# Optimization experiments

Hardware: AMD Instinct MI355X
Metric: run time of the kernel (lower is better)

The kernel has to match this reference:

```python
import jax, jax.numpy as jnp
import numpy as np

N_NODES = 100000
N_EDGES = 3200000
FEAT = 16


def gcn_conv(x, src, dst, W, b):
    # PyG GCNConv: add self-loops, symmetric normalization deg^{-1/2}(A+I)deg^{-1/2},
    # then linear transform and scatter-add aggregation.
    n = x.shape[0]
    loop = jnp.arange(n, dtype=src.dtype)
    s = jnp.concatenate([src, loop])
    d = jnp.concatenate([dst, loop])
    deg = jax.ops.segment_sum(jnp.ones_like(d, dtype=x.dtype), d, num_segments=n)
    dinv = jnp.where(deg > 0, jax.lax.rsqrt(deg), 0.0)
    norm = dinv[s] * dinv[d]  # [E+N]
    h = x @ W  # [N, out]
    msg = h[s] * norm[:, None]  # gather + weight
    out = jax.ops.segment_sum(msg, d, num_segments=n)  # scatter-add
    return out + b


def setup_inputs() -> dict:
    key = jax.random.key(0)
    k1, k2, k3, k4 = jax.random.split(key, 4)
    scale = 1.0 / np.sqrt(FEAT)
    return {
        "x": jax.random.normal(k1, (N_NODES, FEAT), dtype=jnp.float32),
        "edge_index": jax.random.randint(k2, (2, N_EDGES), 0, N_NODES, dtype=jnp.int64) if jax.config.jax_enable_x64 else jax.random.randint(k2, (2, N_EDGES), 0, N_NODES, dtype=jnp.int32),
        "W1": jax.random.normal(k3, (FEAT, 16), dtype=jnp.float32) * scale,
        "b1": jnp.zeros((16,), dtype=jnp.float32),
        "W2": jax.random.normal(k4, (16, FEAT), dtype=jnp.float32) * scale,
        "b2": jnp.zeros((FEAT,), dtype=jnp.float32),
    }


def reference(x, edge_index, W1, b1, W2, b2):
    src, dst = edge_index[0], edge_index[1]
    h = gcn_conv(x, src, dst, W1, b1)
    h = jax.nn.relu(h)
    out = gcn_conv(h, src, dst, W2, b2)
    return out
```

## Files before the change

### kernel.cpp

```cpp
#include <hip/hip_runtime.h>

#define F 16
#define BSHIFT 8
#define NPB 256
#define NB 391
#define CH 4096
#define BCAP 9216


__global__ void init_cursor_kernel(unsigned* __restrict__ cursor) {
    int i = threadIdx.x;
    if (i < NB) cursor[i * 16] = (unsigned)(i * BCAP);
}

__global__ __launch_bounds__(512) void
reorder_kernel(const int* __restrict__ src, const int* __restrict__ dst,
               unsigned* __restrict__ cursor, unsigned* __restrict__ recs, int E) {
    __shared__ unsigned lsorted[CH];
    __shared__ unsigned short lbkt[CH];
    __shared__ unsigned cnt[NB];
    __shared__ unsigned lstart[NB + 1];
    int t = threadIdx.x, b = blockIdx.x;
    int e0 = b * CH;
    int cnt_e = E - e0; if (cnt_e > CH) cnt_e = CH;

    for (int i = t; i < NB; i += 512) cnt[i] = 0;
    __syncthreads();
    unsigned pk[8], rs[8];
#pragma unroll
    for (int j = 0; j < 8; ++j) {
        int i = t + j * 512;
        pk[j] = 0xFFFFFFFFu;
        if (i < cnt_e) {
            unsigned d = (unsigned)dst[e0 + i];
            rs[j] = (unsigned)src[e0 + i];
            unsigned bk = d >> BSHIFT;
            unsigned r = atomicAdd(&cnt[bk], 1u);
            pk[j] = bk | ((d & 255u) << 9) | (r << 17);
        }
    }
    __syncthreads();
    if (t < 64) {
        unsigned run = 0;
        for (int c = 0; c < NB; c += 64) {
            int idx = c + t;
            unsigned v = (idx < NB) ? cnt[idx] : 0u;
            unsigned inc = v;
#pragma unroll
            for (int d = 1; d < 64; d <<= 1) {
                unsigned o = __shfl_up(inc, d, 64);
                if (t >= d) inc += o;
            }
            if (idx < NB) lstart[idx] = run + inc - v;
            run += __shfl(inc, 63, 64);
        }
        if (t == 0) lstart[NB] = (unsigned)cnt_e;
    }
    __syncthreads();
    for (int i = t; i < NB; i += 512) {
        unsigned c = cnt[i];
        if (c) cnt[i] = atomicAdd(&cursor[i * 16], c);
    }
    __syncthreads();
#pragma unroll
    for (int j = 0; j < 8; ++j) {
        int i = t + j * 512;
        if (i < cnt_e) {
            unsigned p = pk[j];
            unsigned bk = p & 0x1FFu;
            unsigned pos = lstart[bk] + (p >> 17);
            lsorted[pos] = rs[j] | (((p >> 9) & 255u) << 17);
            lbkt[pos] = (unsigned short)bk;
        }
    }
    __syncthreads();
    for (int i = t; i < cnt_e; i += 512) {
        unsigned bk = lbkt[i];
        recs[cnt[bk] + ((unsigned)i - lstart[bk])] = lsorted[i];
    }
}

__global__ __launch_bounds__(1024) void
sort2_kernel(const unsigned* __restrict__ recs, const unsigned* __restrict__ cursor,
             unsigned* __restrict__ srcs, int* __restrict__ noff, int* __restrict__ nend,
             float* __restrict__ dinv, const float* __restrict__ x,
             float* __restrict__ z, int n) {
    __shared__ unsigned lsort[BCAP];
    __shared__ unsigned cnt[NPB];
    __shared__ unsigned ex[NPB];
    __shared__ float ldv[NPB];
    __shared__ unsigned wtot[4];
    int t = threadIdx.x, b = blockIdx.x;
    int e0 = b * BCAP;
    int used = (int)(cursor[b * 16] - (unsigned)e0);
    if (t < NPB) cnt[t] = 0;
    __syncthreads();
    unsigned pk[9], rsr[9];
#pragma unroll
    for (int j = 0; j < 9; ++j) {
        int i = t + j * 1024;
        pk[j] = 0xFFFFFFFFu;
        if (i < used) {
            unsigned rec = recs[e0 + i];
            unsigned node = rec >> 17;
            rsr[j] = rec & 0x1FFFFu;
            unsigned r = atomicAdd(&cnt[node], 1u);
            pk[j] = node | (r << 8);
        }
    }
    __syncthreads();
    if (t < NPB) {
        unsigned c = cnt[t];
        unsigned inc = c;
        int lane = t & 63, w = t >> 6;
#pragma unroll
        for (int d = 1; d < 64; d <<= 1) {
            unsigned o = __shfl_up(inc, d, 64);
            if (lane >= d) inc += o;
        }
        if (lane == 63) wtot[w] = inc;
        __syncthreads();
        unsigned wbase = 0;
        for (int i = 0; i < w; ++i) wbase += wtot[i];
        unsigned e = wbase + inc - c;
        ex[t] = e;
        float dv = rsqrtf((float)c + 1.0f);
        ldv[t] = dv;
        int node = b * NPB + t;
        if (node < n) {
            noff[node] = e0 + (int)e;
            nend[node] = e0 + (int)(e + c);
            dinv[node] = dv;
        }
    } else {
        __syncthreads();
    }
    __syncthreads();
#pragma unroll
    for (int j = 0; j < 9; ++j) {
        int i = t + j * 1024;
        if (i < used) {
            unsigned p = pk[j];
            lsort[ex[p & 255u] + (p >> 8)] = rsr[j];
        }
    }
    __syncthreads();
    for (int i = t; i < used; i += 1024) srcs[e0 + i] = lsort[i];
    {
        int node = b * NPB + (t >> 2);
        if (node < n) {
            float4 v = ((const float4*)x)[(size_t)b * 1024 + t];
            float dv = ldv[t >> 2];
            v.x *= dv; v.y *= dv; v.z *= dv; v.w *= dv;
            ((float4*)z)[(size_t)b * 1024 + t] = v;
        }
    }
}

__global__ void agg_csr_kernel(const float* __restrict__ hin, const unsigned* __restrict__ srcs,
                               const int* __restrict__ noff, const int* __restrict__ nend,
                               const float* __restrict__ dinv,
                               const float* __restrict__ W, const float* __restrict__ bias,
                               float* __restrict__ outp, int n, int mode) {
    __shared__ float a1[64][F + 1];
    __shared__ float Ws[F * F];
    int t = threadIdx.x;
    int g = t >> 2, c = t & 3;
    Ws[t] = W[t];
    int node = blockIdx.x * 64 + g;
    const float4* h4 = (const float4*)hin;
    float di = 0.f;
    if (node < n) {
        di = dinv[node];
        int e0 = noff[node], e1 = nend[node];
        float4 s0 = {0,0,0,0}, s1 = {0,0,0,0}, s2 = {0,0,0,0}, s3 = {0,0,0,0};
        int e = e0;
        for (; e + 4 <= e1; e += 4) {
            int ia = srcs[e], ib = srcs[e + 1], ic = srcs[e + 2], id = srcs[e + 3];
            float4 va = h4[(size_t)ia * 4 + c];
            float4 vb = h4[(size_t)ib * 4 + c];
            float4 vc = h4[(size_t)ic * 4 + c];
            float4 vd = h4[(size_t)id * 4 + c];
            s0.x += va.x; s0.y += va.y; s0.z += va.z; s0.w += va.w;
            s1.x += vb.x; s1.y += vb.y; s1.z += vb.z; s1.w += vb.w;
            s2.x += vc.x; s2.y += vc.y; s2.z += vc.z; s2.w += vc.w;
            s3.x += vd.x; s3.y += vd.y; s3.z += vd.z; s3.w += vd.w;
        }
        for (; e < e1; ++e) {
            float4 va = h4[(size_t)srcs[e] * 4 + c];
            s0.x += va.x; s0.y += va.y; s0.z += va.z; s0.w += va.w;
        }
        float4 self = h4[(size_t)node * 4 + c];
        a1[g][c * 4 + 0] = (s0.x + s1.x) + (s2.x + s3.x) + self.x;
        a1[g][c * 4 + 1] = (s0.y + s1.y) + (s2.y + s3.y) + self.y;
        a1[g][c * 4 + 2] = (s0.z + s1.z) + (s2.z + s3.z) + self.z;
        a1[g][c * 4 + 3] = (s0.w + s1.w) + (s2.w + s3.w) + self.w;
    }
    __syncthreads();
    if (node < n) {
        float4 o = {0.f, 0.f, 0.f, 0.f};
        int j = c * 4;
#pragma unroll
        for (int k = 0; k < F; ++k) {
            float ak = a1[g][k];
            o.x += ak * Ws[k * F + j + 0];
            o.y += ak * Ws[k * F + j + 1];
            o.z += ak * Ws[k * F + j + 2];
            o.w += ak * Ws[k * F + j + 3];
        }
        float4 bi = ((const float4*)bias)[c];
        o.x = di * o.x + bi.x; o.y = di * o.y + bi.y;
        o.z = di * o.z + bi.z; o.w = di * o.w + bi.w;
        if (mode == 1) {
            o.x = fmaxf(o.x, 0.f) * di; o.y = fmaxf(o.y, 0.f) * di;
            o.z = fmaxf(o.z, 0.f) * di; o.w = fmaxf(o.w, 0.f) * di;
        }
        ((float4*)outp)[(size_t)node * 4 + c] = o;
    }
}


__global__ void deg_kernel(const int* __restrict__ dst, float* __restrict__ deg, int E) {
    int e = blockIdx.x * blockDim.x + threadIdx.x;
    if (e < E) atomicAdd(&deg[dst[e]], 1.0f);
}
__global__ void dinv_kernel(float* __restrict__ deg, int n) {
    int i = blockIdx.x * blockDim.x + threadIdx.x;
    if (i < n) deg[i] = rsqrtf(deg[i] + 1.0f);
}
__global__ void linear2_kernel(const float* __restrict__ in, const float* __restrict__ acc,
                               const float* __restrict__ dinv, const float* __restrict__ W,
                               const float* __restrict__ bias, float* __restrict__ out,
                               int n, int mode) {
    __shared__ float Ws[F * F];
    __shared__ float As[16][F + 1];
    int t = threadIdx.x;
    Ws[t] = W[t];
    int nb = t >> 4, j = t & 15;
    int i = blockIdx.x * 16 + nb;
    float di = 0.f, v = 0.f;
    if (i < n) {
        di = dinv[i]; v = in[i * F + j];
        if (mode) { v = di * (acc[i * F + j] + v) + bias[j]; v = fmaxf(v, 0.f); }
    }
    As[nb][j] = v;
    __syncthreads();
    if (i < n) {
        float s = 0.f;
#pragma unroll
        for (int k = 0; k < F; ++k) s += As[nb][k] * Ws[k * F + j];
        out[i * F + j] = s * di;
    }
}
__global__ void scatter_kernel(const int* __restrict__ src, const int* __restrict__ dst,
                               const float* __restrict__ h, float* __restrict__ acc, int E) {
    int t = blockIdx.x * blockDim.x + threadIdx.x;
    int e = t >> 4, j = t & 15;
    if (e < E) atomicAdd(&acc[dst[e] * F + j], h[src[e] * F + j]);
}
__global__ void out_kernel(const float* __restrict__ acc, const float* __restrict__ h,
                           const float* __restrict__ dinv, const float* __restrict__ bias,
                           float* __restrict__ out, int n) {
    int t = blockIdx.x * blockDim.x + threadIdx.x;
    if (t < n * F) {
        int i = t >> 4, j = t & 15;
        out[t] = dinv[i] * (acc[t] + h[t]) + bias[j];
    }
}


extern "C" void kernel_launch(void* const* d_in, const int* in_sizes, int n_in,
                              void* d_out, int out_size, void* d_ws, size_t ws_size,
                              hipStream_t stream) {
    const float* x  = (const float*)d_in[0];
    const int*   ei = (const int*)d_in[1];
    const float* W1 = (const float*)d_in[2];
    const float* b1 = (const float*)d_in[3];
    const float* W2 = (const float*)d_in[4];
    const float* b2 = (const float*)d_in[5];
    float* outp = (float*)d_out;

    const int N = in_sizes[0] / F;
    const int E = in_sizes[1] / 2;
    const int* src = ei;
    const int* dst = ei + E;

    const int nb_rt = (N + NPB - 1) >> BSHIFT;
    const size_t RC = (size_t)NB * BCAP;
    size_t need = sizeof(unsigned) * ((size_t)N * 19 + 2 * RC + 16 * NB);

    if (nb_rt == NB && E <= CH * 65535 && ws_size >= need) {
        float* dinv = (float*)d_ws;
        float* z = dinv + N;
        unsigned* recs = (unsigned*)(z + (size_t)F * N);
        float* y = (float*)recs;
        unsigned* srcs = recs + RC;
        int* noff = (int*)(srcs + RC);
        int* nend = noff + N;
        unsigned* cursor = (unsigned*)(nend + N);

        init_cursor_kernel<<<1, 512, 0, stream>>>(cursor);
        reorder_kernel<<<(E + CH - 1) / CH, 512, 0, stream>>>(src, dst, cursor, recs, E);
        sort2_kernel<<<NB, 1024, 0, stream>>>(recs, cursor, srcs, noff, nend, dinv, x, z, N);
        agg_csr_kernel<<<(N + 63) / 64, 256, 0, stream>>>(z, srcs, noff, nend, dinv, W1, b1, y, N, 1);
        agg_csr_kernel<<<(N + 63) / 64, 256, 0, stream>>>(y, srcs, noff, nend, dinv, W2, b2, outp, N, 2);
    } else {
        float* dinv = (float*)d_ws;
        float* h = dinv + N;
        float* acc = h + (size_t)F * N;
        hipMemsetAsync(dinv, 0, (size_t)N * sizeof(float), stream);
        hipMemsetAsync(acc, 0, (size_t)F * N * sizeof(float), stream);
        deg_kernel<<<(E + 255) / 256, 256, 0, stream>>>(dst, dinv, E);
        dinv_kernel<<<(N + 255) / 256, 256, 0, stream>>>(dinv, N);
        linear2_kernel<<<(N + 15) / 16, 256, 0, stream>>>(x, nullptr, dinv, W1, nullptr, h, N, 0);
        scatter_kernel<<<((size_t)E * F + 255) / 256, 256, 0, stream>>>(src, dst, h, acc, E);
        linear2_kernel<<<(N + 15) / 16, 256, 0, stream>>>(h, acc, dinv, W2, b1, h, N, 1);
        hipMemsetAsync(acc, 0, (size_t)F * N * sizeof(float), stream);
        scatter_kernel<<<((size_t)E * F + 255) / 256, 256, 0, stream>>>(src, dst, h, acc, E);
        out_kernel<<<((size_t)N * F + 255) / 256, 256, 0, stream>>>(acc, h, dinv, b2, outp, N);
    }
}
```

Before: 206.3 us.

## Split single-pass bucket scatter into two-level radix partition

Replaces the one-pass bucketing of edges into 391 destination buckets with two passes: first into 13 coarse superbuckets, then each superbucket is split into 32 fine buckets. The aim is to cut the scattered, poorly coalesced global writes and the contention on many cursor atomics that come from spreading each chunk across hundreds of buckets. The cost is an extra kernel launch and an extra full read and write of the edge records, plus workspace buffers reused across stages and fixed capacity assumptions (ACAP) that could overflow on skewed inputs.

```diff
diff --git a/kernel.cpp b/kernel.cpp
--- a/kernel.cpp
+++ b/kernel.cpp
@@ -1,30 +1,36 @@
 #include <hip/hip_runtime.h>
 
 #define F 16
-#define BSHIFT 8
 #define NPB 256
 #define NB 391
-#define CH 4096
 #define BCAP 9216
-
-
-__global__ void init_cursor_kernel(unsigned* __restrict__ cursor) {
+#define NSB 13
+#define SBSHIFT 13
+#define ACAP 270336
+#define CHA 4096
+#define CHB 8192
+#define NBS 32
+
+
+__global__ void init_cursor_kernel(unsigned* __restrict__ cursorA, unsigned* __restrict__ cursorB) {
     int i = threadIdx.x;
-    if (i < NB) cursor[i * 16] = (unsigned)(i * BCAP);
+    if (i < NSB) cursorA[i * 16] = (unsigned)(i * ACAP);
+    if (i < NB)  cursorB[i * 16] = (unsigned)(i * BCAP);
 }
 
 __global__ __launch_bounds__(512) void
-reorder_kernel(const int* __restrict__ src, const int* __restrict__ dst,
-               unsigned* __restrict__ cursor, unsigned* __restrict__ recs, int E) {
-    __shared__ unsigned lsorted[CH];
-    __shared__ unsigned short lbkt[CH];
-    __shared__ unsigned cnt[NB];
-    __shared__ unsigned lstart[NB + 1];
+passA_kernel(const int* __restrict__ src, const int* __restrict__ dst,
+             unsigned* __restrict__ cursorA, unsigned* __restrict__ recsA, int E) {
+    __shared__ unsigned lsorted[CHA];
+    __shared__ unsigned char lbkt[CHA];
+    __shared__ unsigned cnt[NSB];
+    __shared__ unsigned lstart[NSB + 1];
+    __shared__ unsigned base[NSB];
     int t = threadIdx.x, b = blockIdx.x;
-    int e0 = b * CH;
-    int cnt_e = E - e0; if (cnt_e > CH) cnt_e = CH;
-
-    for (int i = t; i < NB; i += 512) cnt[i] = 0;
+    int e0 = b * CHA;
+    int cnt_e = E - e0; if (cnt_e > CHA) cnt_e = CHA;
+    if (cnt_e <= 0) return;
+    if (t < NSB) cnt[t] = 0;
     __syncthreads();
     unsigned pk[8], rs[8];
 #pragma unroll
@@ -34,32 +40,27 @@
         if (i < cnt_e) {
             unsigned d = (unsigned)dst[e0 + i];
             rs[j] = (unsigned)src[e0 + i];
-            unsigned bk = d >> BSHIFT;
+            unsigned bk = d >> SBSHIFT;
             unsigned r = atomicAdd(&cnt[bk], 1u);
-            pk[j] = bk | ((d & 255u) << 9) | (r << 17);
+            pk[j] = bk | ((d & 8191u) << 4) | (r << 17);
         }
     }
     __syncthreads();
     if (t < 64) {
-        unsigned run = 0;
-        for (int c = 0; c < NB; c += 64) {
-            int idx = c + t;
-            unsigned v = (idx < NB) ? cnt[idx] : 0u;
-            unsigned inc = v;
-#pragma unroll
-            for (int d = 1; d < 64; d <<= 1) {
-                unsigned o = __shfl_up(inc, d, 64);
-                if (t >= d) inc += o;
-            }
-            if (idx < NB) lstart[idx] = run + inc - v;
-            run += __shfl(inc, 63, 64);
-        }
-        if (t == 0) lstart[NB] = (unsigned)cnt_e;
-    }
-    __syncthreads();
-    for (int i = t; i < NB; i += 512) {
-        unsigned c = cnt[i];
-        if (c) cnt[i] = atomicAdd(&cursor[i * 16], c);
+        unsigned v = (t < NSB) ? cnt[t] : 0u;
+        unsigned inc = v;
+#pragma unroll
+        for (int d = 1; d < 16; d <<= 1) {
+            unsigned o = __shfl_up(inc, d, 64);
+            if (t >= d) inc += o;
+        }
+        if (t < NSB) lstart[t] = inc - v;
+        if (t == 0) lstart[NSB] = (unsigned)cnt_e;
+    }
+    __syncthreads();
+    if (t < NSB) {
+        unsigned c = cnt[t];
+        base[t] = c ? atomicAdd(&cursorA[t * 16], c) : 0u;
     }
     __syncthreads();
 #pragma unroll
@@ -67,16 +68,85 @@
         int i = t + j * 512;
         if (i < cnt_e) {
             unsigned p = pk[j];
-            unsigned bk = p & 0x1FFu;
+            unsigned bk = p & 15u;
             unsigned pos = lstart[bk] + (p >> 17);
-            lsorted[pos] = rs[j] | (((p >> 9) & 255u) << 17);
-            lbkt[pos] = (unsigned short)bk;
+            lsorted[pos] = rs[j] | (((p >> 4) & 8191u) << 17);
+            lbkt[pos] = (unsigned char)bk;
         }
     }
     __syncthreads();
     for (int i = t; i < cnt_e; i += 512) {
         unsigned bk = lbkt[i];
-        recs[cnt[bk] + ((unsigned)i - lstart[bk])] = lsorted[i];
+        recsA[base[bk] + ((unsigned)i - lstart[bk])] = lsorted[i];
+    }
+}
+
+__global__ __launch_bounds__(1024) void
+passB_kernel(const unsigned* __restrict__ recsA, const unsigned* __restrict__ cursorA,
+             unsigned* __restrict__ cursorB, unsigned* __restrict__ recsB) {
+    __shared__ unsigned lsorted[CHB];
+    __shared__ unsigned char lbkt[CHB];
+    __shared__ unsigned cnt[NBS];
+    __shared__ unsigned lstart[NBS + 1];
+    __shared__ unsigned base[NBS];
+    int t = threadIdx.x;
+    int s = blockIdx.x / (ACAP / CHB);
+    int c = blockIdx.x % (ACAP / CHB);
+    int a0 = s * ACAP;
+    int used = (int)(cursorA[s * 16] - (unsigned)a0);
+    int e0 = c * CHB;
+    int cnt_e = used - e0; if (cnt_e > CHB) cnt_e = CHB;
+    if (cnt_e <= 0) return;
+    if (t < NBS) cnt[t] = 0;
+    __syncthreads();
+    unsigned pk[8], rs[8];
+#pragma unroll
+    for (int j = 0; j < 8; ++j) {
+        int i = t + j * 1024;
+        pk[j] = 0xFFFFFFFFu;
+        if (i < cnt_e) {
+            unsigned rec = recsA[a0 + e0 + i];
+            rs[j] = rec & 0x1FFFFu;
+            unsigned dlow = rec >> 17;
+            unsigned k = dlow >> 8;
+            unsigned r = atomicAdd(&cnt[k], 1u);
+            pk[j] = k | ((dlow & 255u) << 5) | (r << 13);
+        }
+    }
+    __syncthreads();
+    if (t < 64) {
+        unsigned v = (t < NBS) ? cnt[t] : 0u;
+        unsigned inc = v;
+#pragma unroll
+        for (int d = 1; d < 32; d <<= 1) {
+            unsigned o = __shfl_up(inc, d, 64);
+            if (t >= d) inc += o;
+        }
+        if (t < NBS) lstart[t] = inc - v;
+        if (t == 0) lstart[NBS] = (unsigned)cnt_e;
+    }
+    __syncthreads();
+    if (t < NBS) {
+        unsigned cc = cnt[t];
+        int g = s * NBS + t;
+        base[t] = cc ? atomicAdd(&cursorB[g * 16], cc) : 0u;
+    }
+    __syncthreads();
+#pragma unroll
+    for (int j = 0; j < 8; ++j) {
+        int i = t + j * 1024;
+        if (i < cnt_e) {
+            unsigned p = pk[j];
+            unsigned k = p & 31u;
+            unsigned pos = lstart[k] + (p >> 13);
+            lsorted[pos] = rs[j] | (((p >> 5) & 255u) << 17);
+            lbkt[pos] = (unsigned char)k;
+        }
+    }
+    __syncthreads();
+    for (int i = t; i < cnt_e; i += 1024) {
+        unsigned k = lbkt[i];
+        recsB[base[k] + ((unsigned)i - lstart[k])] = lsorted[i];
     }
 }
 
@@ -285,23 +355,28 @@
     const int* src = ei;
     const int* dst = ei + E;
 
-    const int nb_rt = (N + NPB - 1) >> BSHIFT;
+    const int nb_rt = (N + NPB - 1) >> 8;
     const size_t RC = (size_t)NB * BCAP;
-    size_t need = sizeof(unsigned) * ((size_t)N * 19 + 2 * RC + 16 * NB);
-
-    if (nb_rt == NB && E <= CH * 65535 && ws_size >= need) {
+    size_t need = sizeof(unsigned) * ((size_t)N * 19 + 2 * RC + 16 * (NSB + NB));
+
+    if (nb_rt == NB && E <= CHA * 782 && ws_size >= need) {
         float* dinv = (float*)d_ws;
         float* z = dinv + N;
-        unsigned* recs = (unsigned*)(z + (size_t)F * N);
-        float* y = (float*)recs;
-        unsigned* srcs = recs + RC;
-        int* noff = (int*)(srcs + RC);
+        unsigned* regionA = (unsigned*)(z + (size_t)F * N);
+        unsigned* regionB = regionA + RC;
+        int* noff = (int*)(regionB + RC);
         int* nend = noff + N;
-        unsigned* cursor = (unsigned*)(nend + N);
-
-        init_cursor_kernel<<<1, 512, 0, stream>>>(cursor);
-        reorder_kernel<<<(E + CH - 1) / CH, 512, 0, stream>>>(src, dst, cursor, recs, E);
-        sort2_kernel<<<NB, 1024, 0, stream>>>(recs, cursor, srcs, noff, nend, dinv, x, z, N);
+        unsigned* cursorA = (unsigned*)(nend + N);
+        unsigned* cursorB = cursorA + 16 * NSB;
+        unsigned* recsA = regionA;
+        unsigned* srcs  = regionA;
+        unsigned* recsB = regionB;
+        float* y = (float*)regionB;
+
+        init_cursor_kernel<<<1, 512, 0, stream>>>(cursorA, cursorB);
+        passA_kernel<<<(E + CHA - 1) / CHA, 512, 0, stream>>>(src, dst, cursorA, recsA, E);
+        passB_kernel<<<NSB * (ACAP / CHB), 1024, 0, stream>>>(recsA, cursorA, cursorB, recsB);
+        sort2_kernel<<<NB, 1024, 0, stream>>>(recsB, cursorB, srcs, noff, nend, dinv, x, z, N);
         agg_csr_kernel<<<(N + 63) / 64, 256, 0, stream>>>(z, srcs, noff, nend, dinv, W1, b1, y, N, 1);
         agg_csr_kernel<<<(N + 63) / 64, 256, 0, stream>>>(y, srcs, noff, nend, dinv, W2, b2, outp, N, 2);
     } else {
```

Measured after the change: 210.9 us. +2.2%, slower.

## Replace per-node CSR sort with bucketed LDS atomic aggregation

Applied to the files above, without the earlier changes.

Drops the second-level sort that built per-node CSR offsets and source arrays. Degrees come from an LDS histogram in a slimmer kernel. Aggregation runs per 256-node bucket, with 1024-thread blocks scatter-adding gathered features into a shared-memory accumulator through LDS atomics. This removes the sort's writes and its extra workspace, at the cost of many LDS float atomics, run-to-run nondeterministic summation order, and only 391 blocks per aggregation pass.

```diff
diff --git a/kernel.cpp b/kernel.cpp
--- a/kernel.cpp
+++ b/kernel.cpp
@@ -81,128 +81,96 @@
 }
 
 __global__ __launch_bounds__(1024) void
-sort2_kernel(const unsigned* __restrict__ recs, const unsigned* __restrict__ cursor,
-             unsigned* __restrict__ srcs, int* __restrict__ noff, int* __restrict__ nend,
-             float* __restrict__ dinv, const float* __restrict__ x,
-             float* __restrict__ z, int n) {
-    __shared__ unsigned lsort[BCAP];
+degz_kernel(const unsigned* __restrict__ recs, const unsigned* __restrict__ cursor,
+            const float* __restrict__ x, float* __restrict__ dinv,
+            float* __restrict__ z, int n) {
     __shared__ unsigned cnt[NPB];
-    __shared__ unsigned ex[NPB];
     __shared__ float ldv[NPB];
-    __shared__ unsigned wtot[4];
     int t = threadIdx.x, b = blockIdx.x;
     int e0 = b * BCAP;
     int used = (int)(cursor[b * 16] - (unsigned)e0);
     if (t < NPB) cnt[t] = 0;
     __syncthreads();
-    unsigned pk[9], rsr[9];
-#pragma unroll
-    for (int j = 0; j < 9; ++j) {
-        int i = t + j * 1024;
-        pk[j] = 0xFFFFFFFFu;
-        if (i < used) {
-            unsigned rec = recs[e0 + i];
-            unsigned node = rec >> 17;
-            rsr[j] = rec & 0x1FFFFu;
-            unsigned r = atomicAdd(&cnt[node], 1u);
-            pk[j] = node | (r << 8);
-        }
-    }
+    for (int i = t; i < used; i += 1024) atomicAdd(&cnt[recs[e0 + i] >> 17], 1u);
     __syncthreads();
     if (t < NPB) {
-        unsigned c = cnt[t];
-        unsigned inc = c;
-        int lane = t & 63, w = t >> 6;
-#pragma unroll
-        for (int d = 1; d < 64; d <<= 1) {
-            unsigned o = __shfl_up(inc, d, 64);
-            if (lane >= d) inc += o;
-        }
-        if (lane == 63) wtot[w] = inc;
-        __syncthreads();
-        unsigned wbase = 0;
-        for (int i = 0; i < w; ++i) wbase += wtot[i];
-        unsigned e = wbase + inc - c;
-        ex[t] = e;
-        float dv = rsqrtf((float)c + 1.0f);
+        float dv = rsqrtf((float)cnt[t] + 1.0f);
         ldv[t] = dv;
         int node = b * NPB + t;
-        if (node < n) {
-            noff[node] = e0 + (int)e;
-            nend[node] = e0 + (int)(e + c);
-            dinv[node] = dv;
-        }
-    } else {
-        __syncthreads();
-    }
-    __syncthreads();
-#pragma unroll
-    for (int j = 0; j < 9; ++j) {
-        int i = t + j * 1024;
-        if (i < used) {
-            unsigned p = pk[j];
-            lsort[ex[p & 255u] + (p >> 8)] = rsr[j];
-        }
-    }
-    __syncthreads();
-    for (int i = t; i < used; i += 1024) srcs[e0 + i] = lsort[i];
-    {
-        int node = b * NPB + (t >> 2);
-        if (node < n) {
-            float4 v = ((const float4*)x)[(size_t)b * 1024 + t];
-            float dv = ldv[t >> 2];
-            v.x *= dv; v.y *= dv; v.z *= dv; v.w *= dv;
-            ((float4*)z)[(size_t)b * 1024 + t] = v;
-        }
-    }
-}
-
-__global__ void agg_csr_kernel(const float* __restrict__ hin, const unsigned* __restrict__ srcs,
-                               const int* __restrict__ noff, const int* __restrict__ nend,
-                               const float* __restrict__ dinv,
-                               const float* __restrict__ W, const float* __restrict__ bias,
-                               float* __restrict__ outp, int n, int mode) {
-    __shared__ float a1[64][F + 1];
+        if (node < n) dinv[node] = dv;
+    }
+    __syncthreads();
+    int node = b * NPB + (t >> 2);
+    if (node < n) {
+        float4 v = ((const float4*)x)[(size_t)b * 1024 + t];
+        float dv = ldv[t >> 2];
+        v.x *= dv; v.y *= dv; v.z *= dv; v.w *= dv;
+        ((float4*)z)[(size_t)b * 1024 + t] = v;
+    }
+}
+
+__global__ __launch_bounds__(1024) void
+agg_lds_kernel(const float4* __restrict__ hin4, const unsigned* __restrict__ recs,
+               const unsigned* __restrict__ cursor, const float* __restrict__ dinv,
+               const float* __restrict__ W, const float* __restrict__ bias,
+               float4* __restrict__ out4, int n, int mode) {
+    __shared__ float acc[NPB * 17];
     __shared__ float Ws[F * F];
-    int t = threadIdx.x;
+    int t = threadIdx.x, b = blockIdx.x;
+    int e0 = b * BCAP;
+    int used = (int)(cursor[b * 16] - (unsigned)e0);
+    for (int i = t; i < NPB * 17; i += 1024) acc[i] = 0.f;
+    if (t < 256) Ws[t] = W[t];
+    __syncthreads();
     int g = t >> 2, c = t & 3;
-    Ws[t] = W[t];
-    int node = blockIdx.x * 64 + g;
-    const float4* h4 = (const float4*)hin;
-    float di = 0.f;
+    const unsigned* re = recs + e0;
+    int nfull = used >> 10;
+    for (int it = 0; it < nfull; ++it) {
+        int i0 = (it << 10) + g;
+        unsigned r0 = re[i0];
+        unsigned r1 = re[i0 + 256];
+        unsigned r2 = re[i0 + 512];
+        unsigned r3 = re[i0 + 768];
+        float4 v0 = hin4[(size_t)(r0 & 0x1FFFFu) * 4 + c];
+        float4 v1 = hin4[(size_t)(r1 & 0x1FFFFu) * 4 + c];
+        float4 v2 = hin4[(size_t)(r2 & 0x1FFFFu) * 4 + c];
+        float4 v3 = hin4[(size_t)(r3 & 0x1FFFFu) * 4 + c];
+        int a0 = (int)(r0 >> 17) * 17 + c * 4;
+        int a1 = (int)(r1 >> 17) * 17 + c * 4;
+        int a2 = (int)(r2 >> 17) * 17 + c * 4;
+        int a3 = (int)(r3 >> 17) * 17 + c * 4;
+        atomicAdd(&acc[a0 + 0], v0.x); atomicAdd(&acc[a0 + 1], v0.y);
+        atomicAdd(&acc[a0 + 2], v0.z); atomicAdd(&acc[a0 + 3], v0.w);
+        atomicAdd(&acc[a1 + 0], v1.x); atomicAdd(&acc[a1 + 1], v1.y);
+        atomicAdd(&acc[a1 + 2], v1.z); atomicAdd(&acc[a1 + 3], v1.w);
+        atomicAdd(&acc[a2 + 0], v2.x); atomicAdd(&acc[a2 + 1], v2.y);
+        atomicAdd(&acc[a2 + 2], v2.z); atomicAdd(&acc[a2 + 3], v2.w);
+        atomicAdd(&acc[a3 + 0], v3.x); atomicAdd(&acc[a3 + 1], v3.y);
+        atomicAdd(&acc[a3 + 2], v3.z); atomicAdd(&acc[a3 + 3], v3.w);
+    }
+    for (int i = (nfull << 10) + g; i < used; i += 256) {
+        unsigned r = re[i];
+        float4 v = hin4[(size_t)(r & 0x1FFFFu) * 4 + c];
+        int a = (int)(r >> 17) * 17 + c * 4;
+        atomicAdd(&acc[a + 0], v.x); atomicAdd(&acc[a + 1], v.y);
+        atomicAdd(&acc[a + 2], v.z); atomicAdd(&acc[a + 3], v.w);
+    }
+    __syncthreads();
+    int node = b * NPB + g;
     if (node < n) {
-        di = dinv[node];
-        int e0 = noff[node], e1 = nend[node];
-        float4 s0 = {0,0,0,0}, s1 = {0,0,0,0}, s2 = {0,0,0,0}, s3 = {0,0,0,0};
-        int e = e0;
-        for (; e + 4 <= e1; e += 4) {
-            int ia = srcs[e], ib = srcs[e + 1], ic = srcs[e + 2], id = srcs[e + 3];
-            float4 va = h4[(size_t)ia * 4 + c];
-            float4 vb = h4[(size_t)ib * 4 + c];
-            float4 vc = h4[(size_t)ic * 4 + c];
-            float4 vd = h4[(size_t)id * 4 + c];
-            s0.x += va.x; s0.y += va.y; s0.z += va.z; s0.w += va.w;
-            s1.x += vb.x; s1.y += vb.y; s1.z += vb.z; s1.w += vb.w;
-            s2.x += vc.x; s2.y += vc.y; s2.z += vc.z; s2.w += vc.w;
-            s3.x += vd.x; s3.y += vd.y; s3.z += vd.z; s3.w += vd.w;
-        }
-        for (; e < e1; ++e) {
-            float4 va = h4[(size_t)srcs[e] * 4 + c];
-            s0.x += va.x; s0.y += va.y; s0.z += va.z; s0.w += va.w;
-        }
-        float4 self = h4[(size_t)node * 4 + c];
-        a1[g][c * 4 + 0] = (s0.x + s1.x) + (s2.x + s3.x) + self.x;
-        a1[g][c * 4 + 1] = (s0.y + s1.y) + (s2.y + s3.y) + self.y;
-        a1[g][c * 4 + 2] = (s0.z + s1.z) + (s2.z + s3.z) + self.z;
-        a1[g][c * 4 + 3] = (s0.w + s1.w) + (s2.w + s3.w) + self.w;
+        float4 self = hin4[(size_t)node * 4 + c];
+        int a = g * 17 + c * 4;
+        acc[a + 0] += self.x; acc[a + 1] += self.y;
+        acc[a + 2] += self.z; acc[a + 3] += self.w;
     }
     __syncthreads();
     if (node < n) {
+        float di = dinv[node];
         float4 o = {0.f, 0.f, 0.f, 0.f};
         int j = c * 4;
 #pragma unroll
         for (int k = 0; k < F; ++k) {
-            float ak = a1[g][k];
+            float ak = acc[g * 17 + k];
             o.x += ak * Ws[k * F + j + 0];
             o.y += ak * Ws[k * F + j + 1];
             o.z += ak * Ws[k * F + j + 2];
@@ -215,7 +183,7 @@
             o.x = fmaxf(o.x, 0.f) * di; o.y = fmaxf(o.y, 0.f) * di;
             o.z = fmaxf(o.z, 0.f) * di; o.w = fmaxf(o.w, 0.f) * di;
         }
-        ((float4*)outp)[(size_t)node * 4 + c] = o;
+        out4[(size_t)node * 4 + c] = o;
     }
 }
 
@@ -287,23 +255,22 @@
 
     const int nb_rt = (N + NPB - 1) >> BSHIFT;
     const size_t RC = (size_t)NB * BCAP;
-    size_t need = sizeof(unsigned) * ((size_t)N * 19 + 2 * RC + 16 * NB);
-
-    if (nb_rt == NB && E <= CH * 65535 && ws_size >= need) {
+    size_t need = sizeof(unsigned) * ((size_t)N * 33 + RC + 16 * NB);
+
+    if (nb_rt == NB && ws_size >= need) {
         float* dinv = (float*)d_ws;
         float* z = dinv + N;
         unsigned* recs = (unsigned*)(z + (size_t)F * N);
-        float* y = (float*)recs;
-        unsigned* srcs = recs + RC;
-        int* noff = (int*)(srcs + RC);
-        int* nend = noff + N;
-        unsigned* cursor = (unsigned*)(nend + N);
+        float* y = (float*)(recs + RC);
+        unsigned* cursor = (unsigned*)(y + (size_t)F * N);
 
         init_cursor_kernel<<<1, 512, 0, stream>>>(cursor);
         reorder_kernel<<<(E + CH - 1) / CH, 512, 0, stream>>>(src, dst, cursor, recs, E);
-        sort2_kernel<<<NB, 1024, 0, stream>>>(recs, cursor, srcs, noff, nend, dinv, x, z, N);
-        agg_csr_kernel<<<(N + 63) / 64, 256, 0, stream>>>(z, srcs, noff, nend, dinv, W1, b1, y, N, 1);
-        agg_csr_kernel<<<(N + 63) / 64, 256, 0, stream>>>(y, srcs, noff, nend, dinv, W2, b2, outp, N, 2);
+        degz_kernel<<<NB, 1024, 0, stream>>>(recs, cursor, x, dinv, z, N);
+        agg_lds_kernel<<<NB, 1024, 0, stream>>>((const float4*)z, recs, cursor, dinv,
+                                                W1, b1, (float4*)y, N, 1);
+        agg_lds_kernel<<<NB, 1024, 0, stream>>>((const float4*)y, recs, cursor, dinv,
+                                                W2, b2, (float4*)outp, N, 2);
     } else {
         float* dinv = (float*)d_ws;
         float* h = dinv + N;
```

Result: slower. 789.3 us (+282.6%).
